# Optimization experiments

Hardware: AMD Instinct MI355X
Metric: run time of the kernel (lower is better)

Reference implementation:

```python
import jax, jax.numpy as jnp
import numpy as np


def _mlp(x, w1, b1, w2, b2):
    # full_connected / full_connected_conv1d with channels [3,16,32]:
    # pointwise Linear -> LeakyReLU -> Linear (kernel-size-1 conv == linear on last dim)
    h = jax.nn.leaky_relu(x @ w1 + b1)
    return h @ w2 + b2


def setup_inputs() -> dict:
    key = jax.random.key(0)
    ks = jax.random.split(key, 10)
    P, K = 100000, 16            # points, neighbors per point
    C_IN, C_H, C_OUT, C_W = 3, 16, 32, 64
    center = jax.random.normal(ks[0], (P, 1, C_IN), dtype=jnp.float32)
    other = jax.random.normal(ks[1], (P, K, C_IN), dtype=jnp.float32)
    s1 = 1.0 / np.sqrt(C_IN)
    s2 = 1.0 / np.sqrt(C_H)
    # 6 stacked 3->16->32 MLPs: [q, center_k, center_v, other_k, other_v, pos]
    mlp_w1 = jax.random.normal(ks[2], (6, C_IN, C_H), dtype=jnp.float32) * s1
    mlp_b1 = jax.random.normal(ks[3], (6, C_H), dtype=jnp.float32) * s1
    mlp_w2 = jax.random.normal(ks[4], (6, C_H, C_OUT), dtype=jnp.float32) * s2
    mlp_b2 = jax.random.normal(ks[5], (6, C_OUT), dtype=jnp.float32) * s2
    # weight_process: 32->64->32
    wp_w1 = jax.random.normal(ks[6], (C_OUT, C_W), dtype=jnp.float32) / np.sqrt(C_OUT)
    wp_b1 = jax.random.normal(ks[7], (C_W,), dtype=jnp.float32) / np.sqrt(C_OUT)
    wp_w2 = jax.random.normal(ks[8], (C_W, C_OUT), dtype=jnp.float32) / np.sqrt(C_W)
    wp_b2 = jax.random.normal(ks[9], (C_OUT,), dtype=jnp.float32) / np.sqrt(C_W)
    return {"center": center, "other": other,
            "mlp_w1": mlp_w1, "mlp_b1": mlp_b1, "mlp_w2": mlp_w2, "mlp_b2": mlp_b2,
            "wp_w1": wp_w1, "wp_b1": wp_b1, "wp_w2": wp_w2, "wp_b2": wp_b2}


def reference(center, other, mlp_w1, mlp_b1, mlp_w2, mlp_b2, wp_w1, wp_b1, wp_w2, wp_b2):
    # center: [P,1,3], other: [P,K,3]
    q = _mlp(center, mlp_w1[0], mlp_b1[0], mlp_w2[0], mlp_b2[0])      # [P,1,32]
    ck = _mlp(center, mlp_w1[1], mlp_b1[1], mlp_w2[1], mlp_b2[1])     # [P,1,32]
    cv = _mlp(center, mlp_w1[2], mlp_b1[2], mlp_w2[2], mlp_b2[2])     # [P,1,32]
    ok = _mlp(other, mlp_w1[3], mlp_b1[3], mlp_w2[3], mlp_b2[3])      # [P,K,32]
    ov = _mlp(other, mlp_w1[4], mlp_b1[4], mlp_w2[4], mlp_b2[4])      # [P,K,32]
    k_all = jnp.concatenate([ck, ok], axis=-2)                        # [P,K+1,32]
    v_all = jnp.concatenate([cv, ov], axis=-2)                        # [P,K+1,32]
    fea_minus = center - jnp.concatenate([center, other], axis=-2)    # [P,K+1,3]
    pos = _mlp(fea_minus, mlp_w1[5], mlp_b1[5], mlp_w2[5], mlp_b2[5]) # [P,K+1,32]
    fea_weight = _mlp(q - k_all + pos, wp_w1, wp_b1, wp_w2, wp_b2)    # [P,K+1,32]
    # vector attention: softmax over CHANNEL dim (-1), weighted sum over neighbors (-2)
    attn = jax.nn.softmax(fea_weight, axis=-1) * (v_all + pos)
    return jnp.sum(attn, axis=-2)                                     # [P,32]
```

## Files before the change

### kernel.cpp

```cpp
#include <hip/hip_runtime.h>
#include <hip/hip_bf16.h>


constexpr int PPB = 15;

typedef __attribute__((ext_vector_type(8))) short bf8;
typedef __attribute__((ext_vector_type(4))) short bf4;
typedef __attribute__((ext_vector_type(4))) float f4;

__device__ __forceinline__ float lrelu(float v) { return v > 0.f ? v : 0.01f * v; }

__device__ __forceinline__ unsigned int pkbf(float a, float b) {
  const unsigned int ua = __builtin_bit_cast(unsigned int, a) + 0x8000u;
  const unsigned int ub = __builtin_bit_cast(unsigned int, b) + 0x8000u;
  return __builtin_amdgcn_perm(ub, ua, 0x07060302u);
}
__device__ __forceinline__ bf4 mkbf4(float v0, float v1, float v2, float v3) {
  uint2 u; u.x = pkbf(v0, v1); u.y = pkbf(v2, v3);
  return __builtin_bit_cast(bf4, u);
}
__device__ __forceinline__ float bf2f_lo(unsigned int u) {
  return __builtin_bit_cast(float, u << 16);
}
__device__ __forceinline__ float bf2f_hi(unsigned int u) {
  return __builtin_bit_cast(float, u & 0xffff0000u);
}

__device__ __forceinline__ f4 mfma16(bf4 a, bf4 b, f4 c) {
#if __has_builtin(__builtin_amdgcn_mfma_f32_16x16x16_bf16)
  return __builtin_amdgcn_mfma_f32_16x16x16_bf16(a, b, c, 0, 0, 0);
#elif __has_builtin(__builtin_amdgcn_mfma_f32_16x16x16bf16_1k)
  return __builtin_amdgcn_mfma_f32_16x16x16bf16_1k(a, b, c, 0, 0, 0);
#else
  f4 d;
  asm volatile("v_mfma_f32_16x16x16_bf16 %0, %1, %2, %3"
               : "=&v"(d) : "v"(a), "v"(b), "v"(c));
  return d;
#endif
}

__device__ float w1v(const float* mw1, const float* mb1, int s, int k, int n) {
  const int cb = n >> 4, cc = n & 15;
  const int sk = s ? 1 : 3, sv = s ? 2 : 4;
  if (k < 3)  return cb == 0 ? mw1[sk * 48 + k * 16 + cc]
                   : (cb == 1 ? mw1[sv * 48 + k * 16 + cc] : 0.f);
  if (k < 6)  return cb == 2 ? mw1[5 * 48 + (k - 3) * 16 + cc] : 0.f;
  if (k < 9)  return cb == 3 ? mw1[0 * 48 + (k - 6) * 16 + cc] : 0.f;
  if (k == 9) {
    const int m = (cb == 0) ? sk : (cb == 1) ? sv : (cb == 2) ? 5 : 0;
    return mb1[m * 16 + cc];
  }
  return 0.f;
}
__device__ float w2v(const float* mw2, int s, int k, int n) {
  const int sk = s ? 1 : 3, sv = s ? 2 : 4;
  if (n < 32) {
    if (k < 16)            return -mw2[sk * 512 + k * 32 + n];
    if (k >= 32 && k < 48) return  mw2[5 * 512 + (k - 32) * 32 + n];
    if (k >= 48)           return  mw2[0 * 512 + (k - 48) * 32 + n];
    return 0.f;
  } else {
    const int cc = n - 32;
    if (k >= 16 && k < 32) return mw2[sv * 512 + (k - 16) * 32 + cc];
    if (k >= 32 && k < 48) return mw2[5 * 512 + (k - 32) * 32 + cc];
    return 0.f;
  }
}

__global__ void prep_kernel(const float* __restrict__ mw1, const float* __restrict__ mb1,
                            const float* __restrict__ mw2, const float* __restrict__ mb2,
                            const float* __restrict__ ww1, const float* __restrict__ ww2,
                            unsigned short* __restrict__ ws16, float* __restrict__ wsf) {
  const int tid = blockIdx.x * 256 + threadIdx.x;
  const int lane = tid & 63, q = lane >> 4, l = lane & 15;
  if (tid < 512) {
    const int f = tid >> 6, s = f >> 2, c = f & 3;
    for (int j = 0; j < 8; j++)
      ws16[f * 512 + lane * 8 + j] =
          (unsigned short)(pkbf(w1v(mw1, mb1, s, q * 8 + j, c * 16 + l), 0.f) & 0xffffu);
  } else if (tid < 2560) {
    const int f = (tid - 512) >> 6, s = f >> 4, mc = (f >> 2) & 3, kc = f & 3;
    for (int j = 0; j < 4; j++)
      ws16[4096 + f * 256 + lane * 4 + j] =
          (unsigned short)(pkbf(w2v(mw2, s, kc * 16 + q * 4 + j, mc * 16 + l), 0.f) & 0xffffu);
  } else if (tid < 3072) {
    const int f = (tid - 2560) >> 6, mc = f >> 1, kc = f & 1;
    for (int j = 0; j < 4; j++)
      ws16[12288 + f * 256 + lane * 4 + j] =
          (unsigned short)(pkbf(ww1[(kc * 16 + q * 4 + j) * 64 + mc * 16 + l], 0.f) & 0xffffu);
  } else if (tid < 3584) {
    const int f = (tid - 3072) >> 6, mc = f >> 2, kc = f & 3;
    for (int j = 0; j < 4; j++)
      ws16[14336 + f * 256 + lane * 4 + j] =
          (unsigned short)(pkbf(ww2[(kc * 16 + q * 4 + j) * 32 + mc * 16 + l], 0.f) & 0xffffu);
  } else if (tid < 3712) {
    const int t2 = tid - 3584, grp = t2 >> 5, cc = t2 & 31;
    float v;
    if (grp == 0)      v = mb2[cc] - mb2[96 + cc] + mb2[160 + cc];
    else if (grp == 1) v = mb2[128 + cc] + mb2[160 + cc];
    else if (grp == 2) v = mb2[cc] - mb2[32 + cc] + mb2[160 + cc];
    else               v = mb2[64 + cc] + mb2[160 + cc];
    wsf[grp * 32 + cc] = v;
  }
}

__global__ __launch_bounds__(256, 3) void point_attn_kernel(
    const float* __restrict__ center, const float* __restrict__ other,
    const float* __restrict__ wb1, const float* __restrict__ wb2,
    const unsigned short* __restrict__ ws16, const float* __restrict__ wsf,
    float* __restrict__ out, int P) {
  __shared__ float pr[256 * 36];

  const int t = threadIdx.x, lane = t & 63, wv = t >> 6;
  const int q = lane >> 4, l = lane & 15;
  const f4 fzero = {0.f, 0.f, 0.f, 0.f};

  unsigned int d0, d1, d2, d3, d4;
  {
    const int isC = (t >= 240);
    const int pt = isC ? (t - 240) : (t >> 4);
    int p = blockIdx.x * PPB + pt;
    p = p < P ? p : P - 1;
    const float c0 = center[(size_t)p * 3 + 0];
    const float c1 = center[(size_t)p * 3 + 1];
    const float c2 = center[(size_t)p * 3 + 2];
    const float* op = other + ((size_t)p * 16 + (t & 15)) * 3;
    const float o0 = op[0], o1 = op[1], o2 = op[2];
    const float x0 = isC ? c0 : o0, x1 = isC ? c1 : o1, x2 = isC ? c2 : o2;
    const float g0 = c0 - x0, g1 = c1 - x1, g2 = c2 - x2;
    d0 = pkbf(x0, x1); d1 = pkbf(x2, g0); d2 = pkbf(g1, g2);
    d3 = pkbf(c0, c1); d4 = pkbf(c2, 1.0f);
  }

  bf8 W1[4]; bf4 W2[4][4]; f4 bw[2], bvp[2];
  bf4 P1[4][2], P2[2][4];
  unsigned int bp1[4][2], bp2[2][2];

  auto loadSet = [&](int s) {
#pragma unroll
    for (int c = 0; c < 4; c++)
      W1[c] = *(const bf8*)(ws16 + ((s * 4 + c) * 64 + lane) * 8);
#pragma unroll
    for (int mc = 0; mc < 4; mc++)
#pragma unroll
      for (int kc = 0; kc < 4; kc++)
        W2[mc][kc] = *(const bf4*)(ws16 + 4096 + ((s * 16 + mc * 4 + kc) * 64 + lane) * 4);
#pragma unroll
    for (int mc = 0; mc < 2; mc++) {
      bw[mc]  = *(const f4*)(wsf + s * 64 + mc * 16 + q * 4);
      bvp[mc] = *(const f4*)(wsf + s * 64 + 32 + mc * 16 + q * 4);
    }
  };

  loadSet(wv == 3 ? 1 : 0);
#pragma unroll
  for (int mc = 0; mc < 4; mc++)
#pragma unroll
    for (int kc = 0; kc < 2; kc++)
      P1[mc][kc] = *(const bf4*)(ws16 + 12288 + ((mc * 2 + kc) * 64 + lane) * 4);
#pragma unroll
  for (int mc = 0; mc < 2; mc++)
#pragma unroll
    for (int kc = 0; kc < 4; kc++)
      P2[mc][kc] = *(const bf4*)(ws16 + 14336 + ((mc * 4 + kc) * 64 + lane) * 4);
#pragma unroll
  for (int mc = 0; mc < 4; mc++) {
    const f4 b = *(const f4*)(wb1 + mc * 16 + q * 4);
    bp1[mc][0] = pkbf(b[0], b[1]); bp1[mc][1] = pkbf(b[2], b[3]);
  }
#pragma unroll
  for (int mc = 0; mc < 2; mc++) {
    const f4 b = *(const f4*)(wb2 + mc * 16 + q * 4);
    bp2[mc][0] = pkbf(b[0], b[1]); bp2[mc][1] = pkbf(b[2], b[3]);
  }

  auto computeTile = [&](int T) {
    const int src = ((T & 3) << 4) | l;
    const unsigned int s0 = __shfl((int)d0, src), s1 = __shfl((int)d1, src),
                       s2 = __shfl((int)d2, src), s3 = __shfl((int)d3, src),
                       s4 = __shfl((int)d4, src);
    uint4 bu;
    bu.x = q == 0 ? s0 : (q == 1 ? s4 : 0u);
    bu.y = q == 0 ? s1 : 0u;
    bu.z = q == 0 ? s2 : 0u;
    bu.w = q == 0 ? s3 : 0u;
    const bf8 bx = __builtin_bit_cast(bf8, bu);

    bf4 hB[4];
#pragma unroll
    for (int c = 0; c < 4; c++) {
      const f4 D1 = __builtin_amdgcn_mfma_f32_16x16x32_bf16(W1[c], bx, fzero, 0, 0, 0);
      hB[c] = mkbf4(lrelu(D1[0]), lrelu(D1[1]), lrelu(D1[2]), lrelu(D1[3]));
    }

    bf4 wB[2]; float vpv[2][4];
#pragma unroll
    for (int mc = 0; mc < 4; mc++) {
      f4 acc = fzero;
#pragma unroll
      for (int kc = 0; kc < 4; kc++) acc = mfma16(W2[mc][kc], hB[kc], acc);
      if (mc < 2) {
        wB[mc] = mkbf4(acc[0] + bw[mc][0], acc[1] + bw[mc][1],
                       acc[2] + bw[mc][2], acc[3] + bw[mc][3]);
      } else {
#pragma unroll
        for (int j = 0; j < 4; j++) vpv[mc - 2][j] = acc[j] + bvp[mc - 2][j];
      }
    }

    bf4 h2B[4];
#pragma unroll
    for (int mc = 0; mc < 4; mc++) {
      f4 acc = fzero;
#pragma unroll
      for (int kc = 0; kc < 2; kc++) acc = mfma16(P1[mc][kc], wB[kc], acc);
      h2B[mc] = mkbf4(lrelu(acc[0] + bf2f_lo(bp1[mc][0])),
                      lrelu(acc[1] + bf2f_hi(bp1[mc][0])),
                      lrelu(acc[2] + bf2f_lo(bp1[mc][1])),
                      lrelu(acc[3] + bf2f_hi(bp1[mc][1])));
    }

    float fw[2][4];
#pragma unroll
    for (int mc = 0; mc < 2; mc++) {
      f4 acc = fzero;
#pragma unroll
      for (int kc = 0; kc < 4; kc++) acc = mfma16(P2[mc][kc], h2B[kc], acc);
      fw[mc][0] = acc[0] + bf2f_lo(bp2[mc][0]);
      fw[mc][1] = acc[1] + bf2f_hi(bp2[mc][0]);
      fw[mc][2] = acc[2] + bf2f_lo(bp2[mc][1]);
      fw[mc][3] = acc[3] + bf2f_hi(bp2[mc][1]);
    }

    float mx = fw[0][0];
#pragma unroll
    for (int mc = 0; mc < 2; mc++)
#pragma unroll
      for (int j = 0; j < 4; j++) mx = fmaxf(mx, fw[mc][j]);
    mx = fmaxf(mx, __shfl_xor(mx, 16));
    mx = fmaxf(mx, __shfl_xor(mx, 32));
    float e[2][4], sum = 0.f;
#pragma unroll
    for (int mc = 0; mc < 2; mc++)
#pragma unroll
      for (int j = 0; j < 4; j++) { e[mc][j] = __expf(fw[mc][j] - mx); sum += e[mc][j]; }
    sum += __shfl_xor(sum, 16);
    sum += __shfl_xor(sum, 32);
    const float inv = 1.f / sum;

    f4 p0, p1;
#pragma unroll
    for (int j = 0; j < 4; j++) {
      p0[j] = e[0][j] * inv * vpv[0][j];
      p1[j] = e[1][j] * inv * vpv[1][j];
    }
    *(f4*)&pr[(T * 16 + l) * 36 + q * 4] = p0;
    *(f4*)&pr[(T * 16 + l) * 36 + 16 + q * 4] = p1;
  };

  computeTile(wv == 3 ? 15 : wv * 4);
  if (wv == 3) loadSet(0);
  for (int jj = 1; jj < 4; jj++)
    computeTile(wv == 3 ? (11 + jj) : (wv * 4 + jj));

  __syncthreads();

  for (int u = t; u < 480; u += 256) {
    const int pp = u >> 5, c = u & 31;
    float s = pr[(240 + pp) * 36 + c];
#pragma unroll
    for (int r2 = 0; r2 < 16; r2++) s += pr[(pp * 16 + r2) * 36 + c];
    const int gp = blockIdx.x * PPB + pp;
    if (gp < P) out[(size_t)gp * 32 + c] = s;
  }
}

extern "C" void kernel_launch(void* const* d_in, const int* in_sizes, int n_in,
                              void* d_out, int out_size, void* d_ws, size_t ws_size,
                              hipStream_t stream) {
  const float* center = (const float*)d_in[0];
  const float* other  = (const float*)d_in[1];
  unsigned short* ws16 = (unsigned short*)d_ws;
  float* wsf = (float*)((char*)d_ws + 32768);

  prep_kernel<<<15, 256, 0, stream>>>(
      (const float*)d_in[2], (const float*)d_in[3],
      (const float*)d_in[4], (const float*)d_in[5],
      (const float*)d_in[6], (const float*)d_in[8], ws16, wsf);

  const int P = in_sizes[0] / 3;
  const int blocks = (P + PPB - 1) / PPB;
  point_attn_kernel<<<blocks, 256, 0, stream>>>(
      center, other,
      (const float*)d_in[7], (const float*)d_in[9],
      ws16, wsf, (float*)d_out, P);
}
```

Baseline: 155.2 us.

## Fuse weight prep into main kernel, use exp2 softmax and bf16 partials

Removes the separate prep kernel. Every block now builds the packed bf16 weight fragments in shared memory from the raw weights, which saves a launch but repeats that setup work in each of about 6700 blocks. Biases are folded into the MFMA accumulator initialisers. Layer 1 switches from a 16x16x32 MFMA to a 16x16x16 one. Softmax uses exp2 with LOG2E pre-scaled into the second weight matrix and bias, plus a hardware reciprocal. Per-neighbour partials are stored in LDS as bf16, halving LDS traffic at some accuracy cost, and each point's inputs are loaded per tile instead of shuffled.

```diff
diff --git a/kernel.cpp b/kernel.cpp
--- a/kernel.cpp
+++ b/kernel.cpp
@@ -1,20 +1,21 @@
 #include <hip/hip_runtime.h>
-#include <hip/hip_bf16.h>
 
 
 constexpr int PPB = 15;
-
-typedef __attribute__((ext_vector_type(8))) short bf8;
+constexpr float LOG2E = 1.44269504088896340736f;
+
 typedef __attribute__((ext_vector_type(4))) short bf4;
 typedef __attribute__((ext_vector_type(4))) float f4;
 
-__device__ __forceinline__ float lrelu(float v) { return v > 0.f ? v : 0.01f * v; }
-
+__device__ __forceinline__ float lrelu(float v) { return fmaxf(v, 0.01f * v); }
 __device__ __forceinline__ unsigned int pkbf(float a, float b) {
   const unsigned int ua = __builtin_bit_cast(unsigned int, a) + 0x8000u;
   const unsigned int ub = __builtin_bit_cast(unsigned int, b) + 0x8000u;
   return __builtin_amdgcn_perm(ub, ua, 0x07060302u);
 }
+__device__ __forceinline__ unsigned short us16(float a) {
+  return (unsigned short)((__builtin_bit_cast(unsigned int, a) + 0x8000u) >> 16);
+}
 __device__ __forceinline__ bf4 mkbf4(float v0, float v1, float v2, float v3) {
   uint2 u; u.x = pkbf(v0, v1); u.y = pkbf(v2, v3);
   return __builtin_bit_cast(bf4, u);
@@ -25,7 +26,13 @@
 __device__ __forceinline__ float bf2f_hi(unsigned int u) {
   return __builtin_bit_cast(float, u & 0xffff0000u);
 }
-
+__device__ __forceinline__ float exp2fast(float x) {
+#if __has_builtin(__builtin_amdgcn_exp2f)
+  return __builtin_amdgcn_exp2f(x);
+#else
+  float r; asm("v_exp_f32 %0, %1" : "=v"(r) : "v"(x)); return r;
+#endif
+}
 __device__ __forceinline__ f4 mfma16(bf4 a, bf4 b, f4 c) {
 #if __has_builtin(__builtin_amdgcn_mfma_f32_16x16x16_bf16)
   return __builtin_amdgcn_mfma_f32_16x16x16_bf16(a, b, c, 0, 0, 0);
@@ -39,7 +46,8 @@
 #endif
 }
 
-__device__ float w1v(const float* mw1, const float* mb1, int s, int k, int n) {
+__device__ __forceinline__ float w1v(const float* mw1, const float* mb1,
+                                     int s, int k, int n) {
   const int cb = n >> 4, cc = n & 15;
   const int sk = s ? 1 : 3, sv = s ? 2 : 4;
   if (k < 3)  return cb == 0 ? mw1[sk * 48 + k * 16 + cc]
@@ -52,7 +60,7 @@
   }
   return 0.f;
 }
-__device__ float w2v(const float* mw2, int s, int k, int n) {
+__device__ __forceinline__ float w2v(const float* mw2, int s, int k, int n) {
   const int sk = s ? 1 : 3, sv = s ? 2 : 4;
   if (n < 32) {
     if (k < 16)            return -mw2[sk * 512 + k * 32 + n];
@@ -67,88 +75,74 @@
   }
 }
 
-__global__ void prep_kernel(const float* __restrict__ mw1, const float* __restrict__ mb1,
-                            const float* __restrict__ mw2, const float* __restrict__ mb2,
-                            const float* __restrict__ ww1, const float* __restrict__ ww2,
-                            unsigned short* __restrict__ ws16, float* __restrict__ wsf) {
-  const int tid = blockIdx.x * 256 + threadIdx.x;
-  const int lane = tid & 63, q = lane >> 4, l = lane & 15;
-  if (tid < 512) {
-    const int f = tid >> 6, s = f >> 2, c = f & 3;
-    for (int j = 0; j < 8; j++)
-      ws16[f * 512 + lane * 8 + j] =
-          (unsigned short)(pkbf(w1v(mw1, mb1, s, q * 8 + j, c * 16 + l), 0.f) & 0xffffu);
-  } else if (tid < 2560) {
-    const int f = (tid - 512) >> 6, s = f >> 4, mc = (f >> 2) & 3, kc = f & 3;
-    for (int j = 0; j < 4; j++)
-      ws16[4096 + f * 256 + lane * 4 + j] =
-          (unsigned short)(pkbf(w2v(mw2, s, kc * 16 + q * 4 + j, mc * 16 + l), 0.f) & 0xffffu);
-  } else if (tid < 3072) {
-    const int f = (tid - 2560) >> 6, mc = f >> 1, kc = f & 1;
-    for (int j = 0; j < 4; j++)
-      ws16[12288 + f * 256 + lane * 4 + j] =
-          (unsigned short)(pkbf(ww1[(kc * 16 + q * 4 + j) * 64 + mc * 16 + l], 0.f) & 0xffffu);
-  } else if (tid < 3584) {
-    const int f = (tid - 3072) >> 6, mc = f >> 2, kc = f & 3;
-    for (int j = 0; j < 4; j++)
-      ws16[14336 + f * 256 + lane * 4 + j] =
-          (unsigned short)(pkbf(ww2[(kc * 16 + q * 4 + j) * 32 + mc * 16 + l], 0.f) & 0xffffu);
-  } else if (tid < 3712) {
-    const int t2 = tid - 3584, grp = t2 >> 5, cc = t2 & 31;
-    float v;
-    if (grp == 0)      v = mb2[cc] - mb2[96 + cc] + mb2[160 + cc];
-    else if (grp == 1) v = mb2[128 + cc] + mb2[160 + cc];
-    else if (grp == 2) v = mb2[cc] - mb2[32 + cc] + mb2[160 + cc];
-    else               v = mb2[64 + cc] + mb2[160 + cc];
-    wsf[grp * 32 + cc] = v;
-  }
-}
-
 __global__ __launch_bounds__(256, 3) void point_attn_kernel(
     const float* __restrict__ center, const float* __restrict__ other,
-    const float* __restrict__ wb1, const float* __restrict__ wb2,
-    const unsigned short* __restrict__ ws16, const float* __restrict__ wsf,
+    const float* __restrict__ mw1, const float* __restrict__ mb1,
+    const float* __restrict__ mw2, const float* __restrict__ mb2,
+    const float* __restrict__ ww1, const float* __restrict__ wb1,
+    const float* __restrict__ ww2, const float* __restrict__ wb2,
     float* __restrict__ out, int P) {
-  __shared__ float pr[256 * 36];
+  __shared__ unsigned short wt[14336];
+  __shared__ float bs[128];
+  __shared__ unsigned int pr[256 * 20];
 
   const int t = threadIdx.x, lane = t & 63, wv = t >> 6;
   const int q = lane >> 4, l = lane & 15;
-  const f4 fzero = {0.f, 0.f, 0.f, 0.f};
-
-  unsigned int d0, d1, d2, d3, d4;
-  {
-    const int isC = (t >= 240);
-    const int pt = isC ? (t - 240) : (t >> 4);
-    int p = blockIdx.x * PPB + pt;
-    p = p < P ? p : P - 1;
-    const float c0 = center[(size_t)p * 3 + 0];
-    const float c1 = center[(size_t)p * 3 + 1];
-    const float c2 = center[(size_t)p * 3 + 2];
-    const float* op = other + ((size_t)p * 16 + (t & 15)) * 3;
-    const float o0 = op[0], o1 = op[1], o2 = op[2];
-    const float x0 = isC ? c0 : o0, x1 = isC ? c1 : o1, x2 = isC ? c2 : o2;
-    const float g0 = c0 - x0, g1 = c1 - x1, g2 = c2 - x2;
-    d0 = pkbf(x0, x1); d1 = pkbf(x2, g0); d2 = pkbf(g1, g2);
-    d3 = pkbf(c0, c1); d4 = pkbf(c2, 1.0f);
-  }
-
-  bf8 W1[4]; bf4 W2[4][4]; f4 bw[2], bvp[2];
-  bf4 P1[4][2], P2[2][4];
-  unsigned int bp1[4][2], bp2[2][2];
+  const int pbase = blockIdx.x * PPB;
+
+  for (int vt = t; vt < 3712; vt += 256) {
+    const int lv = vt & 63, qv = lv >> 4, lnv = lv & 15;
+    if (vt < 512) {
+      const int f = vt >> 6, s = f >> 2, c = f & 3;
+#pragma unroll
+      for (int j = 0; j < 4; j++)
+        wt[f * 256 + lv * 4 + j] = us16(w1v(mw1, mb1, s, qv * 4 + j, c * 16 + lnv));
+    } else if (vt < 2560) {
+      const int f = (vt - 512) >> 6, s = f >> 4, mc = (f >> 2) & 3, kc = f & 3;
+#pragma unroll
+      for (int j = 0; j < 4; j++)
+        wt[2048 + f * 256 + lv * 4 + j] =
+            us16(w2v(mw2, s, kc * 16 + qv * 4 + j, mc * 16 + lnv));
+    } else if (vt < 3072) {
+      const int f = (vt - 2560) >> 6, mc = f >> 1, kc = f & 1;
+#pragma unroll
+      for (int j = 0; j < 4; j++)
+        wt[10240 + f * 256 + lv * 4 + j] =
+            us16(ww1[(kc * 16 + qv * 4 + j) * 64 + mc * 16 + lnv]);
+    } else if (vt < 3584) {
+      const int f = (vt - 3072) >> 6, mc = f >> 2, kc = f & 3;
+#pragma unroll
+      for (int j = 0; j < 4; j++)
+        wt[12288 + f * 256 + lv * 4 + j] =
+            us16(ww2[(kc * 16 + qv * 4 + j) * 32 + mc * 16 + lnv] * LOG2E);
+    } else {
+      const int t2 = vt - 3584, grp = t2 >> 5, cc = t2 & 31;
+      float v;
+      if (grp == 0)      v = mb2[cc] - mb2[96 + cc] + mb2[160 + cc];
+      else if (grp == 1) v = mb2[128 + cc] + mb2[160 + cc];
+      else if (grp == 2) v = mb2[cc] - mb2[32 + cc] + mb2[160 + cc];
+      else               v = mb2[64 + cc] + mb2[160 + cc];
+      bs[grp * 32 + cc] = v;
+    }
+  }
+  __syncthreads();
+
+  bf4 W1[4], W2[4][4], P1[4][2], P2[2][4];
+  f4 bw[2], bvp[2], b1f[4], b2f[2];
 
   auto loadSet = [&](int s) {
 #pragma unroll
     for (int c = 0; c < 4; c++)
-      W1[c] = *(const bf8*)(ws16 + ((s * 4 + c) * 64 + lane) * 8);
+      W1[c] = *(const bf4*)&wt[(s * 4 + c) * 256 + lane * 4];
 #pragma unroll
     for (int mc = 0; mc < 4; mc++)
 #pragma unroll
       for (int kc = 0; kc < 4; kc++)
-        W2[mc][kc] = *(const bf4*)(ws16 + 4096 + ((s * 16 + mc * 4 + kc) * 64 + lane) * 4);
+        W2[mc][kc] = *(const bf4*)&wt[2048 + (s * 16 + mc * 4 + kc) * 256 + lane * 4];
 #pragma unroll
     for (int mc = 0; mc < 2; mc++) {
-      bw[mc]  = *(const f4*)(wsf + s * 64 + mc * 16 + q * 4);
-      bvp[mc] = *(const f4*)(wsf + s * 64 + 32 + mc * 16 + q * 4);
+      bw[mc]  = *(const f4*)&bs[s * 64 + mc * 16 + q * 4];
+      bvp[mc] = *(const f4*)&bs[s * 64 + 32 + mc * 16 + q * 4];
     }
   };
 
@@ -157,79 +151,80 @@
   for (int mc = 0; mc < 4; mc++)
 #pragma unroll
     for (int kc = 0; kc < 2; kc++)
-      P1[mc][kc] = *(const bf4*)(ws16 + 12288 + ((mc * 2 + kc) * 64 + lane) * 4);
+      P1[mc][kc] = *(const bf4*)&wt[10240 + (mc * 2 + kc) * 256 + lane * 4];
 #pragma unroll
   for (int mc = 0; mc < 2; mc++)
 #pragma unroll
     for (int kc = 0; kc < 4; kc++)
-      P2[mc][kc] = *(const bf4*)(ws16 + 14336 + ((mc * 4 + kc) * 64 + lane) * 4);
-#pragma unroll
-  for (int mc = 0; mc < 4; mc++) {
-    const f4 b = *(const f4*)(wb1 + mc * 16 + q * 4);
-    bp1[mc][0] = pkbf(b[0], b[1]); bp1[mc][1] = pkbf(b[2], b[3]);
-  }
+      P2[mc][kc] = *(const bf4*)&wt[12288 + (mc * 4 + kc) * 256 + lane * 4];
+#pragma unroll
+  for (int mc = 0; mc < 4; mc++) b1f[mc] = *(const f4*)(wb1 + mc * 16 + q * 4);
 #pragma unroll
   for (int mc = 0; mc < 2; mc++) {
     const f4 b = *(const f4*)(wb2 + mc * 16 + q * 4);
-    bp2[mc][0] = pkbf(b[0], b[1]); bp2[mc][1] = pkbf(b[2], b[3]);
-  }
-
-  auto computeTile = [&](int T) {
-    const int src = ((T & 3) << 4) | l;
-    const unsigned int s0 = __shfl((int)d0, src), s1 = __shfl((int)d1, src),
-                       s2 = __shfl((int)d2, src), s3 = __shfl((int)d3, src),
-                       s4 = __shfl((int)d4, src);
-    uint4 bu;
-    bu.x = q == 0 ? s0 : (q == 1 ? s4 : 0u);
-    bu.y = q == 0 ? s1 : 0u;
-    bu.z = q == 0 ? s2 : 0u;
-    bu.w = q == 0 ? s3 : 0u;
-    const bf8 bx = __builtin_bit_cast(bf8, bu);
+#pragma unroll
+    for (int j = 0; j < 4; j++) b2f[mc][j] = b[j] * LOG2E;
+  }
+
+  auto computeTile = [&](int T, bool isC) {
+    float c0, c1, c2, x0, x1, x2, g0, g1, g2;
+    if (isC) {
+      int p = pbase + l; p = p < P ? p : P - 1;
+      c0 = center[(size_t)p * 3 + 0];
+      c1 = center[(size_t)p * 3 + 1];
+      c2 = center[(size_t)p * 3 + 2];
+      x0 = c0; x1 = c1; x2 = c2; g0 = g1 = g2 = 0.f;
+    } else {
+      int p = pbase + T; p = p < P ? p : P - 1;
+      c0 = center[(size_t)p * 3 + 0];
+      c1 = center[(size_t)p * 3 + 1];
+      c2 = center[(size_t)p * 3 + 2];
+      const float* op = other + ((size_t)p * 16 + l) * 3;
+      x0 = op[0]; x1 = op[1]; x2 = op[2];
+      g0 = c0 - x0; g1 = c1 - x1; g2 = c2 - x2;
+    }
+    const unsigned int a0 = pkbf(x0, x1), a1 = pkbf(x2, g0);
+    const unsigned int e0 = pkbf(g1, g2), e1 = pkbf(c0, c1);
+    const unsigned int f0 = pkbf(c2, 1.0f);
+    uint2 bu;
+    bu.x = q == 0 ? a0 : (q == 1 ? e0 : (q == 2 ? f0 : 0u));
+    bu.y = q == 0 ? a1 : (q == 1 ? e1 : 0u);
+    const bf4 bx = __builtin_bit_cast(bf4, bu);
+    const f4 fzero = {0.f, 0.f, 0.f, 0.f};
 
     bf4 hB[4];
 #pragma unroll
     for (int c = 0; c < 4; c++) {
-      const f4 D1 = __builtin_amdgcn_mfma_f32_16x16x32_bf16(W1[c], bx, fzero, 0, 0, 0);
-      hB[c] = mkbf4(lrelu(D1[0]), lrelu(D1[1]), lrelu(D1[2]), lrelu(D1[3]));
-    }
-
-    bf4 wB[2]; float vpv[2][4];
+      const f4 D = mfma16(W1[c], bx, fzero);
+      hB[c] = mkbf4(lrelu(D[0]), lrelu(D[1]), lrelu(D[2]), lrelu(D[3]));
+    }
+
+    bf4 wB[2]; f4 vpv[2];
 #pragma unroll
     for (int mc = 0; mc < 4; mc++) {
-      f4 acc = fzero;
+      f4 acc = (mc < 2) ? bw[mc] : bvp[mc - 2];
 #pragma unroll
       for (int kc = 0; kc < 4; kc++) acc = mfma16(W2[mc][kc], hB[kc], acc);
-      if (mc < 2) {
-        wB[mc] = mkbf4(acc[0] + bw[mc][0], acc[1] + bw[mc][1],
-                       acc[2] + bw[mc][2], acc[3] + bw[mc][3]);
-      } else {
-#pragma unroll
-        for (int j = 0; j < 4; j++) vpv[mc - 2][j] = acc[j] + bvp[mc - 2][j];
-      }
+      if (mc < 2) wB[mc] = mkbf4(acc[0], acc[1], acc[2], acc[3]);
+      else        vpv[mc - 2] = acc;
     }
 
     bf4 h2B[4];
 #pragma unroll
     for (int mc = 0; mc < 4; mc++) {
-      f4 acc = fzero;
+      f4 acc = b1f[mc];
 #pragma unroll
       for (int kc = 0; kc < 2; kc++) acc = mfma16(P1[mc][kc], wB[kc], acc);
-      h2B[mc] = mkbf4(lrelu(acc[0] + bf2f_lo(bp1[mc][0])),
-                      lrelu(acc[1] + bf2f_hi(bp1[mc][0])),
-                      lrelu(acc[2] + bf2f_lo(bp1[mc][1])),
-                      lrelu(acc[3] + bf2f_hi(bp1[mc][1])));
-    }
-
-    float fw[2][4];
+      h2B[mc] = mkbf4(lrelu(acc[0]), lrelu(acc[1]), lrelu(acc[2]), lrelu(acc[3]));
+    }
+
+    f4 fw[2];
 #pragma unroll
     for (int mc = 0; mc < 2; mc++) {
-      f4 acc = fzero;
+      f4 acc = b2f[mc];
 #pragma unroll
       for (int kc = 0; kc < 4; kc++) acc = mfma16(P2[mc][kc], h2B[kc], acc);
-      fw[mc][0] = acc[0] + bf2f_lo(bp2[mc][0]);
-      fw[mc][1] = acc[1] + bf2f_hi(bp2[mc][0]);
-      fw[mc][2] = acc[2] + bf2f_lo(bp2[mc][1]);
-      fw[mc][3] = acc[3] + bf2f_hi(bp2[mc][1]);
+      fw[mc] = acc;
     }
 
     float mx = fw[0][0];
@@ -239,39 +234,58 @@
       for (int j = 0; j < 4; j++) mx = fmaxf(mx, fw[mc][j]);
     mx = fmaxf(mx, __shfl_xor(mx, 16));
     mx = fmaxf(mx, __shfl_xor(mx, 32));
-    float e[2][4], sum = 0.f;
+    float ex[2][4], sum = 0.f;
 #pragma unroll
     for (int mc = 0; mc < 2; mc++)
 #pragma unroll
-      for (int j = 0; j < 4; j++) { e[mc][j] = __expf(fw[mc][j] - mx); sum += e[mc][j]; }
+      for (int j = 0; j < 4; j++) {
+        ex[mc][j] = exp2fast(fw[mc][j] - mx);
+        sum += ex[mc][j];
+      }
     sum += __shfl_xor(sum, 16);
     sum += __shfl_xor(sum, 32);
-    const float inv = 1.f / sum;
+    const float inv = __builtin_amdgcn_rcpf(sum);
 
     f4 p0, p1;
 #pragma unroll
     for (int j = 0; j < 4; j++) {
-      p0[j] = e[0][j] * inv * vpv[0][j];
-      p1[j] = e[1][j] * inv * vpv[1][j];
-    }
-    *(f4*)&pr[(T * 16 + l) * 36 + q * 4] = p0;
-    *(f4*)&pr[(T * 16 + l) * 36 + 16 + q * 4] = p1;
+      p0[j] = ex[0][j] * inv * vpv[0][j];
+      p1[j] = ex[1][j] * inv * vpv[1][j];
+    }
+    const int row = T * 16 + l;
+    uint2 u0, u1;
+    u0.x = pkbf(p0[0], p0[1]); u0.y = pkbf(p0[2], p0[3]);
+    u1.x = pkbf(p1[0], p1[1]); u1.y = pkbf(p1[2], p1[3]);
+    *(uint2*)&pr[row * 20 + 2 * q] = u0;
+    *(uint2*)&pr[row * 20 + 8 + 2 * q] = u1;
   };
 
-  computeTile(wv == 3 ? 15 : wv * 4);
-  if (wv == 3) loadSet(0);
-  for (int jj = 1; jj < 4; jj++)
-    computeTile(wv == 3 ? (11 + jj) : (wv * 4 + jj));
-
+  if (wv == 3) {
+    computeTile(15, true);
+    loadSet(0);
+    computeTile(12, false);
+    computeTile(13, false);
+    computeTile(14, false);
+  } else {
+#pragma unroll
+    for (int jj = 0; jj < 4; jj++) computeTile(wv * 4 + jj, false);
+  }
   __syncthreads();
 
-  for (int u = t; u < 480; u += 256) {
-    const int pp = u >> 5, c = u & 31;
-    float s = pr[(240 + pp) * 36 + c];
-#pragma unroll
-    for (int r2 = 0; r2 < 16; r2++) s += pr[(pp * 16 + r2) * 36 + c];
-    const int gp = blockIdx.x * PPB + pp;
-    if (gp < P) out[(size_t)gp * 32 + c] = s;
+  if (t < 240) {
+    const int pp = t >> 4, cp = t & 15;
+    unsigned int u = pr[(240 + pp) * 20 + cp];
+    float slo = bf2f_lo(u), shi = bf2f_hi(u);
+#pragma unroll
+    for (int r2 = 0; r2 < 16; r2++) {
+      u = pr[(pp * 16 + r2) * 20 + cp];
+      slo += bf2f_lo(u); shi += bf2f_hi(u);
+    }
+    const int gp = pbase + pp;
+    if (gp < P) {
+      float2 o; o.x = slo; o.y = shi;
+      *(float2*)(out + (size_t)gp * 32 + cp * 2) = o;
+    }
   }
 }
 
@@ -280,18 +294,13 @@
                               hipStream_t stream) {
   const float* center = (const float*)d_in[0];
   const float* other  = (const float*)d_in[1];
-  unsigned short* ws16 = (unsigned short*)d_ws;
-  float* wsf = (float*)((char*)d_ws + 32768);
-
-  prep_kernel<<<15, 256, 0, stream>>>(
-      (const float*)d_in[2], (const float*)d_in[3],
-      (const float*)d_in[4], (const float*)d_in[5],
-      (const float*)d_in[6], (const float*)d_in[8], ws16, wsf);
-
   const int P = in_sizes[0] / 3;
   const int blocks = (P + PPB - 1) / PPB;
   point_attn_kernel<<<blocks, 256, 0, stream>>>(
       center, other,
-      (const float*)d_in[7], (const float*)d_in[9],
-      ws16, wsf, (float*)d_out, P);
-}
+      (const float*)d_in[2], (const float*)d_in[3],
+      (const float*)d_in[4], (const float*)d_in[5],
+      (const float*)d_in[6], (const float*)d_in[7],
+      (const float*)d_in[8], (const float*)d_in[9],
+      (float*)d_out, P);
+}
```

Measured after the change: 228.8 us. 47.5% more time.
